# Kernel tuning notes

Hardware: AMD Instinct MI355X
Metric: run time of the kernel (lower is better)

Reference implementation:

```python
import jax, jax.numpy as jnp
import numpy as np

B, Q, K, D, H = 4, 2048, 2048, 512, 8
DH = D // H
MASK_VAL = -1e6


def setup_inputs() -> dict:
    key = jax.random.key(0)
    ks = jax.random.split(key, 8)
    queries = jax.random.normal(ks[0], (B, Q, D), dtype=jnp.float32)
    keys = jax.random.normal(ks[1], (B, K, D), dtype=jnp.float32)
    values = jax.random.normal(ks[2], (B, K, D), dtype=jnp.float32)
    valid_lens = jax.random.randint(ks[3], (B,), 1, K + 1, dtype=jnp.int32)
    # torch nn.Linear weights: shape [out_features, in_features], y = x @ W.T
    s = 1.0 / np.sqrt(D)
    W_q = jax.random.uniform(ks[4], (D, D), jnp.float32, -s, s)
    W_k = jax.random.uniform(ks[5], (D, D), jnp.float32, -s, s)
    W_v = jax.random.uniform(ks[6], (D, D), jnp.float32, -s, s)
    W_o = jax.random.uniform(ks[7], (D, D), jnp.float32, -s, s)
    return {"queries": queries, "keys": keys, "values": values,
            "valid_lens": valid_lens, "W_q": W_q, "W_k": W_k,
            "W_v": W_v, "W_o": W_o}


def _split_heads(x):
    # [B, S, D] -> [B, H, S, DH]
    b, s, _ = x.shape
    return x.reshape(b, s, H, DH).transpose(0, 2, 1, 3)


def reference(queries, keys, values, valid_lens, W_q, W_k, W_v, W_o):
    q = _split_heads(queries @ W_q.T)   # [B,H,Q,DH]
    k = _split_heads(keys @ W_k.T)      # [B,H,K,DH]
    v = _split_heads(values @ W_v.T)    # [B,H,K,DH]
    scores = jnp.einsum("bhqd,bhkd->bhqk", q, k) / jnp.sqrt(jnp.float32(DH))
    # padding mask: key position < valid_len[b], broadcast over heads & queries
    mask = jnp.arange(K)[None, None, None, :] < valid_lens[:, None, None, None]
    scores = jnp.where(mask, scores, MASK_VAL)
    attn = jax.nn.softmax(scores, axis=-1)  # dropout=eval/no-op
    out = jnp.einsum("bhqk,bhkd->bhqd", attn, v)
    out = out.transpose(0, 2, 1, 3).reshape(queries.shape[0], q.shape[2], D)
    return out @ W_o.T
```

## Files before the change

kernel.cpp:

```cpp
#include <hip/hip_runtime.h>
#include <cstdint>
#include <cstddef>

#define BB  4
#define QQ  2048
#define SK  2048
#define DD  512
#define HH  8
#define DHH 64

typedef __bf16 bf16;
typedef bf16  bf16x8 __attribute__((ext_vector_type(8)));
typedef bf16  bf16x4 __attribute__((ext_vector_type(4)));
typedef float f32x4  __attribute__((ext_vector_type(4)));
typedef uint32_t u32x4 __attribute__((ext_vector_type(4)));

__device__ __forceinline__ void async16(void* lds, const void* g) {
  __builtin_amdgcn_global_load_lds(
      (const __attribute__((address_space(1))) unsigned int*)g,
      (__attribute__((address_space(3))) unsigned int*)lds, 16, 0, 0);
}

__device__ __forceinline__ uint32_t pk2(float lo, float hi) {
  return __builtin_amdgcn_perm(__builtin_bit_cast(uint32_t, hi),
                               __builtin_bit_cast(uint32_t, lo), 0x07060302u);
}

__global__ __launch_bounds__(256) void cvt_all(
    const float* __restrict__ q, const float* __restrict__ k,
    const float* __restrict__ v, const float* __restrict__ w0,
    const float* __restrict__ w1, const float* __restrict__ w2,
    const float* __restrict__ w3, bf16* __restrict__ dq,
    bf16* __restrict__ dk, bf16* __restrict__ dv, bf16* __restrict__ dw0,
    bf16* __restrict__ dw1, bf16* __restrict__ dw2, bf16* __restrict__ dw3,
    int nx4, int nw4) {
  int i = blockIdx.x * 256 + threadIdx.x;
  const float* s;
  bf16* d;
  if (i < nx4)               { s = q;  d = dq;  }
  else if (i < 2 * nx4)      { s = k;  d = dk;  i -= nx4; }
  else if (i < 3 * nx4)      { s = v;  d = dv;  i -= 2 * nx4; }
  else {
    int j = i - 3 * nx4;
    if (j < nw4)             { s = w0; d = dw0; }
    else if (j < 2 * nw4)    { s = w1; d = dw1; j -= nw4; }
    else if (j < 3 * nw4)    { s = w2; d = dw2; j -= 2 * nw4; }
    else if (j < 4 * nw4)    { s = w3; d = dw3; j -= 3 * nw4; }
    else return;
    i = j;
  }
  float4 vv = ((const float4*)s)[i];
  bf16x4 o;
  o[0] = (bf16)vv.x; o[1] = (bf16)vv.y; o[2] = (bf16)vv.z; o[3] = (bf16)vv.w;
  ((bf16x4*)d)[i] = o;
}

template <int MT, typename EpiF>
__device__ __forceinline__ void gemm_body(
    const bf16* __restrict__ A, const bf16* __restrict__ B,
    int tM, int tN, EpiF epi_fn) {
  __shared__ __align__(16) bf16 lA[MT * 32 * 64];
  __shared__ __align__(16) bf16 lB[128 * 64];
  const int tid  = threadIdx.x;
  const int l    = tid & 63;
  const int w    = tid >> 6;
  const int lrow = l & 15, lq = l >> 4;
  const int wm = (w >> 1) * (MT * 16), wn = (w & 1) * 64;

  f32x4 acc[MT][4] = {};
  for (int it = 0; it < 8; ++it) {
    const int kt = it * 64;
    if (it) __syncthreads();
#pragma unroll
    for (int j = 0; j < MT; ++j) {
      int c = j * 256 + tid, row = c >> 3, gcc = (c & 7) ^ (row & 7);
      async16(&lA[c * 8], &A[(size_t)(tM + row) * DD + kt + gcc * 8]);
    }
#pragma unroll
    for (int j = 0; j < 4; ++j) {
      int c = j * 256 + tid, row = c >> 3, gcc = (c & 7) ^ (row & 7);
      async16(&lB[c * 8], &B[(size_t)(tN + row) * DD + kt + gcc * 8]);
    }
    __syncthreads();

#pragma unroll
    for (int ks = 0; ks < 2; ++ks) {
      bf16x8 af[MT], bfr[4];
#pragma unroll
      for (int mt = 0; mt < MT; ++mt) {
        int row = wm + mt * 16 + lrow;
        int chunk = row * 8 + ((ks * 4 + lq) ^ (lrow & 7));
        af[mt] = *(const bf16x8*)&lA[chunk * 8];
      }
#pragma unroll
      for (int nt = 0; nt < 4; ++nt) {
        int row = wn + nt * 16 + lrow;
        int chunk = row * 8 + ((ks * 4 + lq) ^ (lrow & 7));
        bfr[nt] = *(const bf16x8*)&lB[chunk * 8];
      }
#pragma unroll
      for (int mt = 0; mt < MT; ++mt)
#pragma unroll
        for (int nt = 0; nt < 4; ++nt)
          acc[mt][nt] = __builtin_amdgcn_mfma_f32_16x16x32_bf16(
              af[mt], bfr[nt], acc[mt][nt], 0, 0, 0);
    }
  }

#pragma unroll
  for (int mt = 0; mt < MT; ++mt)
#pragma unroll
    for (int nt = 0; nt < 4; ++nt) {
      int row0 = tM + wm + mt * 16 + lq * 4;
      int col  = tN + wn + nt * 16 + lrow;
      epi_fn(acc[mt][nt], row0, col);
    }
}

__global__ __launch_bounds__(256, 3) void proj3(
    const bf16* __restrict__ xq, const bf16* __restrict__ wq, bf16* __restrict__ qh,
    const bf16* __restrict__ xk, const bf16* __restrict__ wk, bf16* __restrict__ kh,
    const bf16* __restrict__ xv, const bf16* __restrict__ wv, bf16* __restrict__ vt,
    float qscale) {
  const int z = blockIdx.y, x = blockIdx.x;
  if (z < 2) {
    const bf16* A  = z == 0 ? wq : wk;
    const bf16* B  = z == 0 ? xq : xk;
    bf16* Cout     = z == 0 ? qh : kh;
    const float scale = z == 0 ? qscale : 1.0f;
    int tM = (x & 3) * 128, tN = (x >> 2) * 128;
    gemm_body<4>(A, B, tM, tN, [&](const f32x4& a, int row0, int col) {
      int b2 = col >> 11, s = col & 2047;
      int h2 = row0 >> 6, dh0 = row0 & 63;
      bf16x4 o;
#pragma unroll
      for (int r = 0; r < 4; ++r) o[r] = (bf16)(a[r] * scale);
      *(bf16x4*)&Cout[((size_t)(b2 * HH + h2) * QQ + s) * DHH + dh0] = o;
    });
  } else {
    int tM = (x >> 2) * 128, tN = (x & 3) * 128;
    gemm_body<4>(xv, wv, tM, tN, [&](const f32x4& a, int row0, int col) {
      int b2 = row0 >> 11, s0 = row0 & 2047;
      int h2 = col >> 6,  dh = col & 63;
      int tile = s0 >> 6, kk = s0 & 63;
      int g = kk >> 4, a2 = (kk >> 2) & 3;
      int idx0 = ((g >> 1) * 4 + a2) * 8 + (g & 1) * 4;
      bf16x4 o;
#pragma unroll
      for (int r = 0; r < 4; ++r) o[r] = (bf16)a[r];
      *(bf16x4*)&vt[((size_t)(b2 * HH + h2) * DHH + dh) * SK + tile * 64 + idx0] = o;
    });
  }
}

__global__ __launch_bounds__(256, 3) void proj_o(
    const bf16* __restrict__ wo, const bf16* __restrict__ ao,
    float* __restrict__ Cout) {
  const int x = blockIdx.x;
  int tM = (x & 7) * 64, tN = (x >> 3) * 128;
  gemm_body<2>(wo, ao, tM, tN, [&](const f32x4& a, int row0, int col) {
    *(float4*)&Cout[(size_t)col * DD + row0] = *(const float4*)&a;
  });
}

__global__ __launch_bounds__(256, 3) void attn_fused(
    const bf16* __restrict__ qh, const bf16* __restrict__ kh,
    const bf16* __restrict__ vt, const int* __restrict__ valid_lens,
    bf16* __restrict__ ao) {
  __shared__ __align__(16) bf16 lK[3][64 * 64];
  __shared__ __align__(16) bf16 lV[3][64 * 64];
  const int tid  = threadIdx.x;
  const int l    = tid & 63;
  const int w    = tid >> 6;
  const int lrow = l & 15, lq = l >> 4;
  const int rx   = lrow & 7;
  const int bh = blockIdx.x;
  const int b = bh >> 3, h = bh & 7;
  const int qt = blockIdx.y;
  const int vl  = valid_lens[b];
  const int nkt = (vl + 63) >> 6;

  const int q0 = qt * 128 + w * 32;
  const bf16* qbase = qh + (size_t)bh * QQ * DHH;
  const bf16* kbase = kh + (size_t)bh * SK * DHH;
  const bf16* vbase = vt + (size_t)bh * DHH * SK;

  auto stageKV = [&](int k0, int buf) {
#pragma unroll
    for (int j = 0; j < 2; ++j) {
      int c = j * 256 + tid, row = c >> 3, gcc = (c & 7) ^ (row & 7);
      async16(&lK[buf][c * 8], &kbase[(size_t)(k0 + row) * DHH + gcc * 8]);
    }
#pragma unroll
    for (int j = 0; j < 2; ++j) {
      int c = j * 256 + tid, row = c >> 3, gcc = (c & 7) ^ (row & 7);
      async16(&lV[buf][c * 8], &vbase[(size_t)row * SK + k0 + gcc * 8]);
    }
  };

  bf16x8 qf[2][2];
#pragma unroll
  for (int g = 0; g < 2; ++g)
#pragma unroll
    for (int ks = 0; ks < 2; ++ks)
      qf[g][ks] = *(const bf16x8*)
          &qbase[(size_t)(q0 + g * 16 + lrow) * DHH + ks * 32 + lq * 8];

  f32x4 acc[2][4] = {};
  float rs[2] = {0.f, 0.f};

  stageKV(0, 0);
  asm volatile("s_waitcnt vmcnt(0)" ::: "memory");

  for (int kt = 0; kt < nkt; ++kt) {
    const int bi = kt % 3;
    if (kt + 1 < nkt) {
      stageKV((kt + 1) * 64, (kt + 1) % 3);
      asm volatile("s_waitcnt vmcnt(4)" ::: "memory");
    } else {
      asm volatile("s_waitcnt vmcnt(0)" ::: "memory");
    }
    __builtin_amdgcn_s_barrier();
    asm volatile("" ::: "memory");
    const bf16* bufK = lK[bi];
    const bf16* bufV = lV[bi];
    const int k0 = kt * 64;

    f32x4 s[2][4] = {};
#pragma unroll
    for (int ks = 0; ks < 2; ++ks) {
#pragma unroll
      for (int t = 0; t < 4; ++t) {
        int row = t * 16 + lrow;
        int chunkc = row * 8 + ((ks * 4 + lq) ^ rx);
        bf16x8 kf = *(const bf16x8*)&bufK[chunkc * 8];
#pragma unroll
        for (int g = 0; g < 2; ++g)
          s[g][t] = __builtin_amdgcn_mfma_f32_16x16x32_bf16(
              kf, qf[g][ks], s[g][t], 0, 0, 0);
      }
    }

    if (vl < k0 + 64) {
#pragma unroll
      for (int t = 0; t < 4; ++t) {
        int kb = k0 + t * 16 + lq * 4;
#pragma unroll
        for (int r = 0; r < 4; ++r)
          if (kb + r >= vl) { s[0][t][r] = -1e30f; s[1][t][r] = -1e30f; }
      }
    }

#pragma unroll
    for (int g = 0; g < 2; ++g)
#pragma unroll
      for (int t = 0; t < 4; ++t)
#pragma unroll
        for (int r = 0; r < 4; ++r) {
          float p = __builtin_amdgcn_exp2f(s[g][t][r]);
          rs[g] += p;
          s[g][t][r] = p;
        }

#pragma unroll
    for (int p2 = 0; p2 < 2; ++p2) {
      u32x4 pu[2];
#pragma unroll
      for (int g = 0; g < 2; ++g) {
        pu[g][0] = pk2(s[g][2 * p2][0], s[g][2 * p2][1]);
        pu[g][1] = pk2(s[g][2 * p2][2], s[g][2 * p2][3]);
        pu[g][2] = pk2(s[g][2 * p2 + 1][0], s[g][2 * p2 + 1][1]);
        pu[g][3] = pk2(s[g][2 * p2 + 1][2], s[g][2 * p2 + 1][3]);
      }
      bf16x8 pb0 = __builtin_bit_cast(bf16x8, pu[0]);
      bf16x8 pb1 = __builtin_bit_cast(bf16x8, pu[1]);
      int cc = (p2 * 4 + lq) ^ rx;
#pragma unroll
      for (int mt = 0; mt < 4; ++mt) {
        int row = mt * 16 + lrow;
        bf16x8 vf = *(const bf16x8*)&bufV[(row * 8 + cc) * 8];
        acc[0][mt] = __builtin_amdgcn_mfma_f32_16x16x32_bf16(
            vf, pb0, acc[0][mt], 0, 0, 0);
        acc[1][mt] = __builtin_amdgcn_mfma_f32_16x16x32_bf16(
            vf, pb1, acc[1][mt], 0, 0, 0);
      }
    }
  }

#pragma unroll
  for (int g = 0; g < 2; ++g) {
    rs[g] += __shfl_xor(rs[g], 16);
    rs[g] += __shfl_xor(rs[g], 32);
  }

#pragma unroll
  for (int g = 0; g < 2; ++g) {
    float inv = 1.0f / rs[g];
    int q = q0 + g * 16 + lrow;
#pragma unroll
    for (int mt = 0; mt < 4; ++mt) {
      bf16x4 o;
#pragma unroll
      for (int r = 0; r < 4; ++r) o[r] = (bf16)(acc[g][mt][r] * inv);
      *(bf16x4*)&ao[((size_t)(b * QQ + q)) * DD + h * DHH + mt * 16 + lq * 4] = o;
    }
  }
}

extern "C" void kernel_launch(void* const* d_in, const int* in_sizes, int n_in,
                              void* d_out, int out_size, void* d_ws, size_t ws_size,
                              hipStream_t stream) {
  const float* queries    = (const float*)d_in[0];
  const float* keys       = (const float*)d_in[1];
  const float* values     = (const float*)d_in[2];
  const int*   valid_lens = (const int*)d_in[3];
  const float* W_q = (const float*)d_in[4];
  const float* W_k = (const float*)d_in[5];
  const float* W_v = (const float*)d_in[6];
  const float* W_o = (const float*)d_in[7];

  const size_t NX = (size_t)BB * QQ * DD;
  const size_t NW = (size_t)DD * DD;

  bf16* xq = (bf16*)d_ws;
  bf16* xk = xq + NX;
  bf16* xv = xk + NX;
  bf16* wq = xv + NX;
  bf16* wk = wq + NW;
  bf16* wv = wk + NW;
  bf16* wo = wv + NW;
  bf16* qh = wo + NW;
  bf16* kh = qh + NX;
  bf16* vt = kh + NX;
  bf16* ao = xq;

  dim3 blk(256);
  const int nx4 = (int)(NX / 4), nw4 = (int)(NW / 4);
  const int ncvt = (3 * nx4 + 4 * nw4 + 255) / 256;
  cvt_all<<<dim3(ncvt), blk, 0, stream>>>(
      queries, keys, values, W_q, W_k, W_v, W_o,
      xq, xk, xv, wq, wk, wv, wo, nx4, nw4);

  const float qscale = 0.125f * 1.44269504088896340736f;
  proj3<<<dim3(256, 3), blk, 0, stream>>>(xq, wq, qh, xk, wk, kh, xv, wv, vt,
                                          qscale);

  attn_fused<<<dim3(BB * HH, QQ / 128), blk, 0, stream>>>(
      qh, kh, vt, valid_lens, ao);

  proj_o<<<dim3(512), blk, 0, stream>>>(wo, ao, (float*)d_out);
}
```

Measured before the change: 175.9 us.

## Fuse fp32-to-bf16 activation conversion into projection GEMM staging; add MFMA priority hints

The separate conversion pass over the three fp32 activation tensors is removed. The projection GEMM now loads the fp32 activations into registers one k-tile ahead, converts them to bf16 and writes them into the swizzled LDS tile, while the weights still use async global-to-LDS loads. This drops a full write and read of the bf16 activation copies, at the cost of more registers and synchronous register-to-LDS stores inside the GEMM loop. The attention kernel also raises wave priority (s_setprio) around its MFMA blocks to favour matrix-core issue.

```diff
diff --git a/kernel.cpp b/kernel.cpp
--- a/kernel.cpp
+++ b/kernel.cpp
@@ -26,39 +26,31 @@
                                __builtin_bit_cast(uint32_t, lo), 0x07060302u);
 }
 
-__global__ __launch_bounds__(256) void cvt_all(
-    const float* __restrict__ q, const float* __restrict__ k,
-    const float* __restrict__ v, const float* __restrict__ w0,
-    const float* __restrict__ w1, const float* __restrict__ w2,
-    const float* __restrict__ w3, bf16* __restrict__ dq,
-    bf16* __restrict__ dk, bf16* __restrict__ dv, bf16* __restrict__ dw0,
-    bf16* __restrict__ dw1, bf16* __restrict__ dw2, bf16* __restrict__ dw3,
-    int nx4, int nw4) {
+__global__ __launch_bounds__(256) void cvt_w(
+    const float* __restrict__ w0, const float* __restrict__ w1,
+    const float* __restrict__ w2, const float* __restrict__ w3,
+    bf16* __restrict__ d0, bf16* __restrict__ d1, bf16* __restrict__ d2,
+    bf16* __restrict__ d3, int nw4) {
   int i = blockIdx.x * 256 + threadIdx.x;
   const float* s;
   bf16* d;
-  if (i < nx4)               { s = q;  d = dq;  }
-  else if (i < 2 * nx4)      { s = k;  d = dk;  i -= nx4; }
-  else if (i < 3 * nx4)      { s = v;  d = dv;  i -= 2 * nx4; }
-  else {
-    int j = i - 3 * nx4;
-    if (j < nw4)             { s = w0; d = dw0; }
-    else if (j < 2 * nw4)    { s = w1; d = dw1; j -= nw4; }
-    else if (j < 3 * nw4)    { s = w2; d = dw2; j -= 2 * nw4; }
-    else if (j < 4 * nw4)    { s = w3; d = dw3; j -= 3 * nw4; }
-    else return;
-    i = j;
-  }
+  if (i < nw4)             { s = w0; d = d0; }
+  else if (i < 2 * nw4)    { s = w1; d = d1; i -= nw4; }
+  else if (i < 3 * nw4)    { s = w2; d = d2; i -= 2 * nw4; }
+  else if (i < 4 * nw4)    { s = w3; d = d3; i -= 3 * nw4; }
+  else return;
   float4 vv = ((const float4*)s)[i];
   bf16x4 o;
   o[0] = (bf16)vv.x; o[1] = (bf16)vv.y; o[2] = (bf16)vv.z; o[3] = (bf16)vv.w;
   ((bf16x4*)d)[i] = o;
 }
 
-template <int MT, typename EpiF>
+template <int MT, int F32S, typename EpiF>
 __device__ __forceinline__ void gemm_body(
     const bf16* __restrict__ A, const bf16* __restrict__ B,
+    const float* __restrict__ Af, const float* __restrict__ Bf,
     int tM, int tN, EpiF epi_fn) {
+  static_assert(F32S == 0 || MT == 4, "f32 staging assumes 4 chunks/thread");
   __shared__ __align__(16) bf16 lA[MT * 32 * 64];
   __shared__ __align__(16) bf16 lB[128 * 64];
   const int tid  = threadIdx.x;
@@ -67,21 +59,56 @@
   const int lrow = l & 15, lq = l >> 4;
   const int wm = (w >> 1) * (MT * 16), wn = (w & 1) * 64;
 
+  float4 rg[8];
+  auto loadreg = [&](int it) {
+    const int kt = it * 64;
+#pragma unroll
+    for (int j = 0; j < 4; ++j) {
+      int c = j * 256 + tid, row = c >> 3, gcc = (c & 7) ^ (row & 7);
+      const float* s = (F32S == 1)
+          ? &Af[(size_t)(tM + row) * DD + kt + gcc * 8]
+          : &Bf[(size_t)(tN + row) * DD + kt + gcc * 8];
+      rg[2 * j]     = *(const float4*)s;
+      rg[2 * j + 1] = *(const float4*)(s + 4);
+    }
+  };
+  auto writereg = [&]() {
+#pragma unroll
+    for (int j = 0; j < 4; ++j) {
+      int c = j * 256 + tid;
+      float4 a = rg[2 * j], b2 = rg[2 * j + 1];
+      bf16x8 o;
+      o[0] = (bf16)a.x;  o[1] = (bf16)a.y;  o[2] = (bf16)a.z;  o[3] = (bf16)a.w;
+      o[4] = (bf16)b2.x; o[5] = (bf16)b2.y; o[6] = (bf16)b2.z; o[7] = (bf16)b2.w;
+      if constexpr (F32S == 1) *(bf16x8*)&lA[c * 8] = o;
+      else                     *(bf16x8*)&lB[c * 8] = o;
+    }
+  };
+
   f32x4 acc[MT][4] = {};
+  if constexpr (F32S) loadreg(0);
   for (int it = 0; it < 8; ++it) {
     const int kt = it * 64;
     if (it) __syncthreads();
-#pragma unroll
-    for (int j = 0; j < MT; ++j) {
-      int c = j * 256 + tid, row = c >> 3, gcc = (c & 7) ^ (row & 7);
-      async16(&lA[c * 8], &A[(size_t)(tM + row) * DD + kt + gcc * 8]);
-    }
-#pragma unroll
-    for (int j = 0; j < 4; ++j) {
-      int c = j * 256 + tid, row = c >> 3, gcc = (c & 7) ^ (row & 7);
-      async16(&lB[c * 8], &B[(size_t)(tN + row) * DD + kt + gcc * 8]);
-    }
+    if constexpr (F32S != 1) {
+#pragma unroll
+      for (int j = 0; j < MT; ++j) {
+        int c = j * 256 + tid, row = c >> 3, gcc = (c & 7) ^ (row & 7);
+        async16(&lA[c * 8], &A[(size_t)(tM + row) * DD + kt + gcc * 8]);
+      }
+    }
+    if constexpr (F32S != 2) {
+#pragma unroll
+      for (int j = 0; j < 4; ++j) {
+        int c = j * 256 + tid, row = c >> 3, gcc = (c & 7) ^ (row & 7);
+        async16(&lB[c * 8], &B[(size_t)(tN + row) * DD + kt + gcc * 8]);
+      }
+    }
+    if constexpr (F32S) writereg();
     __syncthreads();
+    if constexpr (F32S) {
+      if (it + 1 < 8) loadreg(it + 1);
+    }
 
 #pragma unroll
     for (int ks = 0; ks < 2; ++ks) {
@@ -118,18 +145,19 @@
 }
 
 __global__ __launch_bounds__(256, 3) void proj3(
-    const bf16* __restrict__ xq, const bf16* __restrict__ wq, bf16* __restrict__ qh,
-    const bf16* __restrict__ xk, const bf16* __restrict__ wk, bf16* __restrict__ kh,
-    const bf16* __restrict__ xv, const bf16* __restrict__ wv, bf16* __restrict__ vt,
+    const float* __restrict__ xq, const bf16* __restrict__ wq, bf16* __restrict__ qh,
+    const float* __restrict__ xk, const bf16* __restrict__ wk, bf16* __restrict__ kh,
+    const float* __restrict__ xv, const bf16* __restrict__ wv, bf16* __restrict__ vt,
     float qscale) {
   const int z = blockIdx.y, x = blockIdx.x;
   if (z < 2) {
-    const bf16* A  = z == 0 ? wq : wk;
-    const bf16* B  = z == 0 ? xq : xk;
+    const bf16*  A = z == 0 ? wq : wk;
+    const float* Bf = z == 0 ? xq : xk;
     bf16* Cout     = z == 0 ? qh : kh;
     const float scale = z == 0 ? qscale : 1.0f;
     int tM = (x & 3) * 128, tN = (x >> 2) * 128;
-    gemm_body<4>(A, B, tM, tN, [&](const f32x4& a, int row0, int col) {
+    gemm_body<4, 2>(A, nullptr, nullptr, Bf, tM, tN,
+                    [&](const f32x4& a, int row0, int col) {
       int b2 = col >> 11, s = col & 2047;
       int h2 = row0 >> 6, dh0 = row0 & 63;
       bf16x4 o;
@@ -139,7 +167,8 @@
     });
   } else {
     int tM = (x >> 2) * 128, tN = (x & 3) * 128;
-    gemm_body<4>(xv, wv, tM, tN, [&](const f32x4& a, int row0, int col) {
+    gemm_body<4, 1>(nullptr, wv, xv, nullptr, tM, tN,
+                    [&](const f32x4& a, int row0, int col) {
       int b2 = row0 >> 11, s0 = row0 & 2047;
       int h2 = col >> 6,  dh = col & 63;
       int tile = s0 >> 6, kk = s0 & 63;
@@ -158,7 +187,8 @@
     float* __restrict__ Cout) {
   const int x = blockIdx.x;
   int tM = (x & 7) * 64, tN = (x >> 3) * 128;
-  gemm_body<2>(wo, ao, tM, tN, [&](const f32x4& a, int row0, int col) {
+  gemm_body<2, 0>(wo, ao, nullptr, nullptr, tM, tN,
+                  [&](const f32x4& a, int row0, int col) {
     *(float4*)&Cout[(size_t)col * DD + row0] = *(const float4*)&a;
   });
 }
@@ -227,6 +257,7 @@
     const int k0 = kt * 64;
 
     f32x4 s[2][4] = {};
+    __builtin_amdgcn_s_setprio(1);
 #pragma unroll
     for (int ks = 0; ks < 2; ++ks) {
 #pragma unroll
@@ -240,6 +271,7 @@
               kf, qf[g][ks], s[g][t], 0, 0, 0);
       }
     }
+    __builtin_amdgcn_s_setprio(0);
 
     if (vl < k0 + 64) {
 #pragma unroll
@@ -275,6 +307,7 @@
       bf16x8 pb0 = __builtin_bit_cast(bf16x8, pu[0]);
       bf16x8 pb1 = __builtin_bit_cast(bf16x8, pu[1]);
       int cc = (p2 * 4 + lq) ^ rx;
+      __builtin_amdgcn_s_setprio(1);
 #pragma unroll
       for (int mt = 0; mt < 4; ++mt) {
         int row = mt * 16 + lrow;
@@ -284,6 +317,7 @@
         acc[1][mt] = __builtin_amdgcn_mfma_f32_16x16x32_bf16(
             vf, pb1, acc[1][mt], 0, 0, 0);
       }
+      __builtin_amdgcn_s_setprio(0);
     }
   }
 
@@ -322,28 +356,23 @@
   const size_t NX = (size_t)BB * QQ * DD;
   const size_t NW = (size_t)DD * DD;
 
-  bf16* xq = (bf16*)d_ws;
-  bf16* xk = xq + NX;
-  bf16* xv = xk + NX;
-  bf16* wq = xv + NX;
+  bf16* wq = (bf16*)d_ws;
   bf16* wk = wq + NW;
   bf16* wv = wk + NW;
   bf16* wo = wv + NW;
   bf16* qh = wo + NW;
   bf16* kh = qh + NX;
   bf16* vt = kh + NX;
-  bf16* ao = xq;
+  bf16* ao = vt + NX;
 
   dim3 blk(256);
-  const int nx4 = (int)(NX / 4), nw4 = (int)(NW / 4);
-  const int ncvt = (3 * nx4 + 4 * nw4 + 255) / 256;
-  cvt_all<<<dim3(ncvt), blk, 0, stream>>>(
-      queries, keys, values, W_q, W_k, W_v, W_o,
-      xq, xk, xv, wq, wk, wv, wo, nx4, nw4);
+  const int nw4 = (int)(NW / 4);
+  cvt_w<<<dim3((4 * nw4 + 255) / 256), blk, 0, stream>>>(
+      W_q, W_k, W_v, W_o, wq, wk, wv, wo, nw4);
 
   const float qscale = 0.125f * 1.44269504088896340736f;
-  proj3<<<dim3(256, 3), blk, 0, stream>>>(xq, wq, qh, xk, wk, kh, xv, wv, vt,
-                                          qscale);
+  proj3<<<dim3(256, 3), blk, 0, stream>>>(queries, wq, qh, keys, wk, kh,
+                                          values, wv, vt, qscale);
 
   attn_fused<<<dim3(BB * HH, QQ / 128), blk, 0, stream>>>(
       qh, kh, vt, valid_lens, ao);
```

Result: slower. 185.0 us (+5.2%).
